# Kernel optimization log

Hardware: AMD Instinct MI355X
Metric: run time of the kernel (lower is better)

Reference implementation:

```python
import jax, jax.numpy as jnp
import numpy as np

N_HEADS = 16
ROPE_BASE = 10000.0
EPS = float(np.finfo(np.float32).eps)  # F.rms_norm default eps for fp32


def _rms_norm(x):
    # RMSNorm over last dim, no learned scale (modded-nanogpt `norm`)
    return x * jax.lax.rsqrt(jnp.mean(jnp.square(x), axis=-1, keepdims=True) + EPS)


def _rotary(x):
    # x: [B, T, H, D]; non-interleaved half-rotation as in the Rotary module
    B, T, H, D = x.shape
    inv_freq = (1.0 / ROPE_BASE) ** (jnp.arange(0, D, 2, dtype=jnp.float32) / D)  # [D/2]
    t = jnp.arange(T, dtype=jnp.float32)
    freqs = jnp.outer(t, inv_freq)  # [T, D/2]
    cos = jnp.cos(freqs)[None, :, None, :]
    sin = jnp.sin(freqs)[None, :, None, :]
    x1, x2 = jnp.split(x, 2, axis=3)
    y1 = x1 * cos + x2 * sin
    y2 = -x1 * sin + x2 * cos
    return jnp.concatenate((y1, y2), axis=3).astype(x.dtype)


def setup_inputs() -> dict:
    key = jax.random.key(0)
    k1, k2, k3, k4 = jax.random.split(key, 4)
    B, T, Hs = 1, 2048, 2048
    d_head = Hs // N_HEADS
    std = 0.5 * d_head ** (-0.5)
    bound = 3 ** 0.5 * std
    x = jax.random.normal(k1, (B, T, Hs), dtype=jnp.float32)
    Wqkv = jax.random.uniform(k2, (3, Hs, Hs), dtype=jnp.float32, minval=-bound, maxval=bound)
    Wo_w = jax.random.normal(k3, (Hs, Hs), dtype=jnp.float32) * (Hs ** -0.5)
    Wo_b = jax.random.normal(k4, (Hs,), dtype=jnp.float32) * 0.01
    return {"x": x, "Wqkv": Wqkv, "Wo_w": Wo_w, "Wo_b": Wo_b}


def reference(x, Wqkv, Wo_w, Wo_b):
    B, T, Hs = x.shape
    d_head = Hs // N_HEADS
    # fused QKV projection: F.linear(x, Wqkv.flatten(end_dim=1)) -> x @ W^T
    W = Wqkv.reshape(3 * Hs, Hs)
    qkv = jnp.einsum('bth,oh->bto', x, W).reshape(B, T, 3 * N_HEADS, d_head)
    q, k, v = jnp.split(qkv, 3, axis=-2)  # each [B, T, H, D]
    q, k = _rms_norm(q), _rms_norm(k)
    q, k = _rotary(q), _rotary(k)
    # causal attention (flex_attention block_mask = causal), scale = 1/sqrt(d)
    scale = 1.0 / jnp.sqrt(jnp.float32(d_head))
    scores = jnp.einsum('bthd,bshd->bhts', q, k) * scale  # [B, H, T, S]
    causal = jnp.tril(jnp.ones((T, T), dtype=bool))
    scores = jnp.where(causal[None, None], scores, jnp.float32(-1e30))
    probs = jax.nn.softmax(scores, axis=-1)
    y = jnp.einsum('bhts,bshd->bthd', probs, v).reshape(B, T, Hs)
    return jnp.einsum('bth,oh->bto', y, Wo_w) + Wo_b
```

## Files before the change

kernel.cpp:

```cpp
#include <hip/hip_runtime.h>
#include <hip/hip_bf16.h>
#include <stdint.h>

#define T_SEQ 2048
#define HS    2048
#define NH    16
#define DH    128
#define QKVN  (3*HS)

typedef __attribute__((ext_vector_type(8))) short          bf16x8;
typedef __attribute__((ext_vector_type(4))) float          f32x4;
typedef __attribute__((ext_vector_type(4))) unsigned short us4;
typedef __attribute__((ext_vector_type(8))) unsigned short us8;

__device__ __forceinline__ unsigned short f2bf(float x) {
  unsigned int u = __float_as_uint(x);
  return (unsigned short)((u + 0x7fffu + ((u >> 16) & 1u)) >> 16);
}

__device__ __forceinline__ void gl_lds16(const void* g, void* l) {
  __builtin_amdgcn_global_load_lds((__attribute__((address_space(1))) void*)g,
                                   (__attribute__((address_space(3))) void*)l, 16, 0, 0);
}

__global__ __launch_bounds__(256) void cast_bf16_kernel(const float* __restrict__ in,
                                                        unsigned short* __restrict__ out, int n) {
  int i = (blockIdx.x * 256 + threadIdx.x) * 8;
  if (i >= n) return;
  f32x4 a = *(const f32x4*)(in + i);
  f32x4 b = *(const f32x4*)(in + i + 4);
  us8 r;
#pragma unroll
  for (int j = 0; j < 4; ++j) { r[j] = f2bf(a[j]); r[j + 4] = f2bf(b[j]); }
  *(us8*)(out + i) = r;
}

__global__ __launch_bounds__(256) void rope_table_kernel(float* __restrict__ cosd,
                                                         float* __restrict__ sind) {
  int i = blockIdx.x * 256 + threadIdx.x;
  if (i >= T_SEQ * 64) return;
  int t = i >> 6, f = i & 63;
  float inv = expf(-9.210340371976184f * (float)f * (1.0f / 64.0f));
  float ang = (float)t * inv;
  float s, c;
  sincosf(ang, &s, &c);
  cosd[i] = c; sind[i] = s;
}

template <int BIAS, int BN>
__global__ __launch_bounds__(256, 4)
void gemm_bt(const unsigned short* __restrict__ A, const unsigned short* __restrict__ Bt,
             float* __restrict__ C, const float* __restrict__ bias, int M, int N, int K) {
  constexpr int FN = BN / 32;
  __shared__ unsigned short As[128 * 64];
  __shared__ unsigned short Bs[BN * 64];
  const int tid  = threadIdx.x;
  const int lane = tid & 63;
  const int w    = tid >> 6;
  const int fr   = lane & 15;
  const int fq   = lane >> 4;
  const int bm   = blockIdx.y * 128;
  const int bn   = blockIdx.x * BN;
  const int wr   = (w >> 1) * 64;
  const int wc   = (w & 1) * (BN / 2);

  f32x4 acc[4][FN];
#pragma unroll
  for (int m = 0; m < 4; ++m)
#pragma unroll
    for (int n = 0; n < FN; ++n) { acc[m][n][0]=0.f; acc[m][n][1]=0.f; acc[m][n][2]=0.f; acc[m][n][3]=0.f; }

  const int srow = lane >> 3;
  const int sg   = (lane & 7) ^ srow;
  const unsigned short* Ag = A + (long)bm * K;
  const unsigned short* Bg = Bt + (long)bn * K;

  const int nk = K >> 6;
  for (int kt = 0; kt < nk; ++kt) {
    const int k0 = kt << 6;
    __syncthreads();
#pragma unroll
    for (int i = 0; i < 4; ++i) {
      int r = i * 32 + w * 8;
      gl_lds16(Ag + (long)(r + srow) * K + k0 + sg * 8, &As[r * 64]);
    }
#pragma unroll
    for (int i = 0; i < BN / 32; ++i) {
      int r = i * 32 + w * 8;
      gl_lds16(Bg + (long)(r + srow) * K + k0 + sg * 8, &Bs[r * 64]);
    }
    __syncthreads();
    __builtin_amdgcn_s_setprio(1);
#pragma unroll
    for (int ks = 0; ks < 2; ++ks) {
      bf16x8 af[4], bfr[FN];
#pragma unroll
      for (int m = 0; m < 4; ++m)
        af[m]  = *(const bf16x8*)&As[(wr + m * 16 + fr) * 64 + (((ks * 4 + fq) ^ (fr & 7)) << 3)];
#pragma unroll
      for (int n = 0; n < FN; ++n)
        bfr[n] = *(const bf16x8*)&Bs[(wc + n * 16 + fr) * 64 + (((ks * 4 + fq) ^ (fr & 7)) << 3)];
#pragma unroll
      for (int m = 0; m < 4; ++m)
#pragma unroll
        for (int n = 0; n < FN; ++n)
          acc[m][n] = __builtin_amdgcn_mfma_f32_16x16x32_bf16(af[m], bfr[n], acc[m][n], 0, 0, 0);
    }
    __builtin_amdgcn_s_setprio(0);
  }
#pragma unroll
  for (int m = 0; m < 4; ++m) {
    int row0 = bm + wr + m * 16 + fq * 4;
#pragma unroll
    for (int n = 0; n < FN; ++n) {
      int col = bn + wc + n * 16 + fr;
      float bv = BIAS ? bias[col] : 0.0f;
#pragma unroll
      for (int j = 0; j < 4; ++j)
        C[(long)(row0 + j) * N + col] = acc[m][n][j] + bv;
    }
  }
}

__global__ __launch_bounds__(256)
void normrope_qk(const float* __restrict__ qkv, const float* __restrict__ cosd,
                 const float* __restrict__ sind, unsigned short* __restrict__ qb,
                 unsigned short* __restrict__ kb) {
  const int wgl  = (blockIdx.x * 256 + threadIdx.x) >> 6;
  const int lane = threadIdx.x & 63;
  for (int rr = wgl; rr < T_SEQ * 32; rr += 4096) {
    const int t = rr >> 5;
    const int y = rr & 31;
    const float2 v = *(const float2*)(qkv + (long)t * QKVN + y * 128 + lane * 2);
    float ss = v.x * v.x + v.y * v.y;
#pragma unroll
    for (int m = 1; m < 64; m <<= 1) ss += __shfl_xor(ss, m, 64);
    const float r = rsqrtf(ss * (1.0f / 128.0f) + 1.1920928955078125e-07f);
    const float a = v.x * r, b = v.y * r;
    const float pa = __shfl_xor(a, 32, 64), pb = __shfl_xor(b, 32, 64);
    const float2 c2 = *(const float2*)(cosd + t * 64 + (lane & 31) * 2);
    const float2 s2 = *(const float2*)(sind + t * 64 + (lane & 31) * 2);
    float o0, o1;
    if (lane < 32) { o0 =  a * c2.x + pa * s2.x;  o1 =  b * c2.y + pb * s2.y; }
    else           { o0 = -pa * s2.x + a * c2.x;  o1 = -pb * s2.y + b * c2.y; }
    unsigned short* dst = (y >> 4) ? kb : qb;
    const unsigned int packed = (unsigned int)f2bf(o0) | ((unsigned int)f2bf(o1) << 16);
    *(unsigned int*)(dst + ((long)(y & 15) * T_SEQ + t) * 128 + lane * 2) = packed;
  }
}

__global__ __launch_bounds__(256)
void v_transpose(const float* __restrict__ qkv, unsigned short* __restrict__ vt) {
  const int tb = blockIdx.x;
  const int h  = blockIdx.y;
  __shared__ unsigned short vl[128][72];
  const int tid = threadIdx.x;
#pragma unroll
  for (int p = 0; p < 32; ++p) {
    int rr = p * 2 + (tid >> 7);
    int d  = tid & 127;
    float x = qkv[(long)(tb * 64 + rr) * QKVN + 2 * HS + h * 128 + d];
    vl[d][rr] = f2bf(x);
  }
  __syncthreads();
#pragma unroll
  for (int p = 0; p < 8; ++p) {
    int idx = (p * 256 + tid) * 4;
    int d = idx >> 6;
    int i = idx & 63;
    us4 val = *(const us4*)&vl[d][i];
    *(us4*)&vt[((long)h * DH + d) * T_SEQ + tb * 64 + i] = val;
  }
}

__global__ __launch_bounds__(256, 2)
void attn_kernel(const unsigned short* __restrict__ qg, const unsigned short* __restrict__ kg,
                 const unsigned short* __restrict__ vtg, float* __restrict__ accG,
                 float* __restrict__ mlG) {
  const int bi = blockIdx.x;
  const int q0 = (bi & 255) >> 4;
  const int h  = bi & 15;
  const int quarter = bi >> 8;
  const int qb = (quarter < 2) ? (31 - q0) : q0;
  const int p  = quarter & 1;
  const int slot = (qb * 16 + h) * 2 + p;

  const int kt0 = p ? ((qb >> 1) + 1) : 0;
  const int kte = p ? qb : (qb >> 1);

  const int tid = threadIdx.x, lane = tid & 63, w = tid >> 6;
  const int fr = lane & 15, fq = lane >> 4;

  float* accO = accG + (long)slot * 8192;
  float* mlO  = mlG + slot * 128;

  if (kt0 > kte) {
#pragma unroll
    for (int j3 = 0; j3 < 4; ++j3) {
      int row = w * 16 + fq * 4 + j3;
      if (fr == 0) { mlO[row] = -1e30f; mlO[64 + row] = 0.f; }
    }
    return;
  }

  __shared__ unsigned short Ks[2][64 * 128];
  __shared__ unsigned short Vts[2][128 * 64];
  __shared__ unsigned short Ps[4][16 * 72];

  const unsigned short* qh = qg  + (long)h * T_SEQ * 128;
  const unsigned short* kh = kg  + (long)h * T_SEQ * 128;
  const unsigned short* vh = vtg + (long)h * 128 * T_SEQ;

  const int krow_off = lane >> 4;
  const int vrow_off = lane >> 3;
  const int vg       = (lane & 7) ^ vrow_off;

  {
    const unsigned short* ksrc = kh + (long)kt0 * 8192;
#pragma unroll
    for (int i = 0; i < 4; ++i) {
      int c = w * 4 + i;
      int r = 4 * c + krow_off;
      int gr = (lane & 15) ^ (r & 7);
      gl_lds16(ksrc + r * 128 + gr * 8, &Ks[0][c * 512]);
    }
#pragma unroll
    for (int i = 0; i < 4; ++i) {
      int r0 = (w * 4 + i) * 8;
      gl_lds16(vh + (long)(r0 + vrow_off) * T_SEQ + kt0 * 64 + vg * 8, &Vts[0][r0 * 64]);
    }
  }

  bf16x8 aq[4];
  {
    const unsigned short* qrow = qh + (long)(qb * 64 + w * 16 + fr) * 128;
#pragma unroll
    for (int ks = 0; ks < 4; ++ks)
      aq[ks] = *(const bf16x8*)(qrow + ks * 32 + fq * 8);
  }

  f32x4 acc[8];
#pragma unroll
  for (int n = 0; n < 8; ++n) { acc[n][0]=0.f; acc[n][1]=0.f; acc[n][2]=0.f; acc[n][3]=0.f; }
  float mrow[4], lrow[4];
#pragma unroll
  for (int j2 = 0; j2 < 4; ++j2) { mrow[j2] = -1e30f; lrow[j2] = 0.f; }

  const float scale = 0.08838834764831845f;

  __syncthreads();

  for (int kt = kt0; kt <= kte; ++kt) {
    const int cur = (kt - kt0) & 1;

    if (kt < kte) {
      const int nb = cur ^ 1;
      const unsigned short* ksrc = kh + (long)(kt + 1) * 8192;
#pragma unroll
      for (int i = 0; i < 4; ++i) {
        int c = w * 4 + i;
        int r = 4 * c + krow_off;
        int gr = (lane & 15) ^ (r & 7);
        gl_lds16(ksrc + r * 128 + gr * 8, &Ks[nb][c * 512]);
      }
#pragma unroll
      for (int i = 0; i < 4; ++i) {
        int r0 = (w * 4 + i) * 8;
        gl_lds16(vh + (long)(r0 + vrow_off) * T_SEQ + (kt + 1) * 64 + vg * 8, &Vts[nb][r0 * 64]);
      }
    }

    f32x4 sv[4];
#pragma unroll
    for (int n = 0; n < 4; ++n) { sv[n][0]=0.f; sv[n][1]=0.f; sv[n][2]=0.f; sv[n][3]=0.f; }
    __builtin_amdgcn_s_setprio(1);
#pragma unroll
    for (int ks = 0; ks < 4; ++ks)
#pragma unroll
      for (int n = 0; n < 4; ++n) {
        int R = n * 16 + fr;
        bf16x8 bk = *(const bf16x8*)&Ks[cur][R * 128 + (((ks * 4 + fq) ^ (fr & 7)) << 3)];
        sv[n] = __builtin_amdgcn_mfma_f32_16x16x32_bf16(aq[ks], bk, sv[n], 0, 0, 0);
      }
    __builtin_amdgcn_s_setprio(0);

#pragma unroll
    for (int n = 0; n < 4; ++n)
#pragma unroll
      for (int j3 = 0; j3 < 4; ++j3) {
        float s = sv[n][j3] * scale;
        if (kt == qb && (n * 16 + fr) > (w * 16 + fq * 4 + j3)) s = -1e30f;
        sv[n][j3] = s;
      }

    float pm[4];
#pragma unroll
    for (int j3 = 0; j3 < 4; ++j3)
      pm[j3] = fmaxf(fmaxf(sv[0][j3], sv[1][j3]), fmaxf(sv[2][j3], sv[3][j3]));
#pragma unroll
    for (int m = 1; m < 16; m <<= 1)
#pragma unroll
      for (int j3 = 0; j3 < 4; ++j3) pm[j3] = fmaxf(pm[j3], __shfl_xor(pm[j3], m, 64));

    float alpha[4];
#pragma unroll
    for (int j3 = 0; j3 < 4; ++j3) {
      float mn = fmaxf(mrow[j3], pm[j3]);
      alpha[j3] = __expf(mrow[j3] - mn);
      mrow[j3] = mn;
    }
    float rs[4] = {0.f, 0.f, 0.f, 0.f};
#pragma unroll
    for (int n = 0; n < 4; ++n)
#pragma unroll
      for (int j3 = 0; j3 < 4; ++j3) {
        float pval = __expf(sv[n][j3] - mrow[j3]);
        sv[n][j3] = pval;
        rs[j3] += pval;
      }
#pragma unroll
    for (int m = 1; m < 16; m <<= 1)
#pragma unroll
      for (int j3 = 0; j3 < 4; ++j3) rs[j3] += __shfl_xor(rs[j3], m, 64);
#pragma unroll
    for (int j3 = 0; j3 < 4; ++j3) lrow[j3] = lrow[j3] * alpha[j3] + rs[j3];
#pragma unroll
    for (int n = 0; n < 8; ++n)
#pragma unroll
      for (int j3 = 0; j3 < 4; ++j3) acc[n][j3] *= alpha[j3];

    unsigned short* pl = &Ps[w][0];
#pragma unroll
    for (int n = 0; n < 4; ++n)
#pragma unroll
      for (int j3 = 0; j3 < 4; ++j3)
        pl[(fq * 4 + j3) * 72 + n * 16 + fr] = f2bf(sv[n][j3]);
    asm volatile("s_waitcnt lgkmcnt(0)" ::: "memory");
    __builtin_amdgcn_s_setprio(1);
#pragma unroll
    for (int ks = 0; ks < 2; ++ks) {
      bf16x8 pa = *(const bf16x8*)&pl[fr * 72 + ks * 32 + fq * 8];
#pragma unroll
      for (int n = 0; n < 8; ++n) {
        int R = n * 16 + fr;
        bf16x8 bv = *(const bf16x8*)&Vts[cur][R * 64 + (((ks * 4 + fq) ^ (fr & 7)) << 3)];
        acc[n] = __builtin_amdgcn_mfma_f32_16x16x32_bf16(pa, bv, acc[n], 0, 0, 0);
      }
    }
    __builtin_amdgcn_s_setprio(0);

    __syncthreads();
  }

#pragma unroll
  for (int j3 = 0; j3 < 4; ++j3) {
    int row = w * 16 + fq * 4 + j3;
#pragma unroll
    for (int n = 0; n < 8; ++n)
      accO[row * 128 + n * 16 + fr] = acc[n][j3];
    if (fr == 0) { mlO[row] = mrow[j3]; mlO[64 + row] = lrow[j3]; }
  }
}

__global__ __launch_bounds__(256)
void attn_combine(const float* __restrict__ accG, const float* __restrict__ mlG,
                  unsigned short* __restrict__ yb) {
  const int j = blockIdx.x;
  const int qb = j >> 4, h = j & 15;
  const float* a0 = accG + (long)(j * 2 + 0) * 8192;
  const float* a1 = accG + (long)(j * 2 + 1) * 8192;
  const float* ml0 = mlG + (j * 2 + 0) * 128;
  const float* ml1 = mlG + (j * 2 + 1) * 128;
  const int tid = threadIdx.x;
#pragma unroll
  for (int e = 0; e < 8; ++e) {
    int idx = e * 256 + tid;
    int row = idx >> 5;
    int c4  = (idx & 31) * 4;
    float m0 = ml0[row], l0 = ml0[64 + row];
    float m1 = ml1[row], l1 = ml1[64 + row];
    float m  = fmaxf(m0, m1);
    float w0 = __expf(m0 - m), w1 = __expf(m1 - m);
    float inv = 1.0f / (l0 * w0 + l1 * w1);
    f32x4 A = *(const f32x4*)(a0 + row * 128 + c4);
    f32x4 B = *(const f32x4*)(a1 + row * 128 + c4);
    us4 o;
#pragma unroll
    for (int q = 0; q < 4; ++q)
      o[q] = f2bf((A[q] * w0 + B[q] * w1) * inv);
    *(us4*)(yb + (long)(qb * 64 + row) * HS + h * 128 + c4) = o;
  }
}

extern "C" void kernel_launch(void* const* d_in, const int* in_sizes, int n_in,
                              void* d_out, int out_size, void* d_ws, size_t ws_size,
                              hipStream_t stream) {
  const float* x    = (const float*)d_in[0];
  const float* Wqkv = (const float*)d_in[1];
  const float* Wo_w = (const float*)d_in[2];
  const float* Wo_b = (const float*)d_in[3];
  float* out = (float*)d_out;
  char* ws = (char*)d_ws;

  unsigned short* xbf  = (unsigned short*)(ws + 0L);
  unsigned short* wqbf = (unsigned short*)(ws + 8388608L);
  unsigned short* wobf = (unsigned short*)(ws + 33554432L);
  float*          qkv  = (float*)         (ws + 41943040L);
  unsigned short* qb   = (unsigned short*)(ws + 92274688L);
  unsigned short* kb   = (unsigned short*)(ws + 100663296L);
  unsigned short* vt   = (unsigned short*)(ws + 109051904L);
  unsigned short* yb   = (unsigned short*)(ws + 117440512L);
  float*          cosd = (float*)         (ws + 125829120L);
  float*          sind = (float*)         (ws + 126353408L);
  float*          accG = (float*)         (ws + 0L);
  float*          mlG  = (float*)         (ws + 41943040L);

  cast_bf16_kernel<<<dim3(4194304 / 8 / 256), 256, 0, stream>>>(x, xbf, 4194304);
  cast_bf16_kernel<<<dim3(12582912 / 8 / 256), 256, 0, stream>>>(Wqkv, wqbf, 12582912);
  cast_bf16_kernel<<<dim3(4194304 / 8 / 256), 256, 0, stream>>>(Wo_w, wobf, 4194304);
  rope_table_kernel<<<dim3(512), 256, 0, stream>>>(cosd, sind);

  gemm_bt<0, 128><<<dim3(QKVN / 128, T_SEQ / 128), 256, 0, stream>>>(xbf, wqbf, qkv, nullptr,
                                                                     T_SEQ, QKVN, HS);
  normrope_qk<<<dim3(1024), 256, 0, stream>>>(qkv, cosd, sind, qb, kb);
  v_transpose<<<dim3(T_SEQ / 64, NH), 256, 0, stream>>>(qkv, vt);
  attn_kernel<<<dim3(1024), 256, 0, stream>>>(qb, kb, vt, accG, mlG);
  attn_combine<<<dim3(512), 256, 0, stream>>>(accG, mlG, yb);
  gemm_bt<1, 64><<<dim3(HS / 64, T_SEQ / 128), 256, 0, stream>>>(yb, wobf, out, Wo_b,
                                                                 T_SEQ, HS, HS);
}
```

Before: 289.1 us.

## Compute softmax row sums via MFMA, use exp2, skip rescale when max unchanged

Folds log2(e) into the score scale so every exponential becomes exp2f, and the combine kernel now uses base-2 weights to match. The row-sum shuffle reduction is replaced by an extra MFMA of the bf16 probabilities against a vector of ones, accumulating the normalizer in accS. The acc/alpha rescaling is wrapped in a wave-uniform branch that runs only when some row max grows. This removes shuffle reductions and VALU work from the softmax inner loop, at the cost of an extra MFMA per k-step and a normalizer summed from bf16-rounded probabilities.

```diff
diff --git a/kernel.cpp b/kernel.cpp
--- a/kernel.cpp
+++ b/kernel.cpp
@@ -239,14 +239,19 @@
       aq[ks] = *(const bf16x8*)(qrow + ks * 32 + fq * 8);
   }
 
+  bf16x8 vone;
+#pragma unroll
+  for (int e = 0; e < 8; ++e) vone[e] = (short)0x3F80;
+
   f32x4 acc[8];
 #pragma unroll
   for (int n = 0; n < 8; ++n) { acc[n][0]=0.f; acc[n][1]=0.f; acc[n][2]=0.f; acc[n][3]=0.f; }
-  float mrow[4], lrow[4];
-#pragma unroll
-  for (int j2 = 0; j2 < 4; ++j2) { mrow[j2] = -1e30f; lrow[j2] = 0.f; }
-
-  const float scale = 0.08838834764831845f;
+  f32x4 accS;  accS[0]=0.f; accS[1]=0.f; accS[2]=0.f; accS[3]=0.f;
+  float mrow[4];
+#pragma unroll
+  for (int j2 = 0; j2 < 4; ++j2) mrow[j2] = -1e30f;
+
+  const float scale2 = 0.08838834764831845f * 1.4426950408889634f;
 
   __syncthreads();
 
@@ -288,7 +293,7 @@
     for (int n = 0; n < 4; ++n)
 #pragma unroll
       for (int j3 = 0; j3 < 4; ++j3) {
-        float s = sv[n][j3] * scale;
+        float s = sv[n][j3] * scale2;
         if (kt == qb && (n * 16 + fr) > (w * 16 + fq * 4 + j3)) s = -1e30f;
         sv[n][j3] = s;
       }
@@ -302,44 +307,35 @@
 #pragma unroll
       for (int j3 = 0; j3 < 4; ++j3) pm[j3] = fmaxf(pm[j3], __shfl_xor(pm[j3], m, 64));
 
-    float alpha[4];
-#pragma unroll
-    for (int j3 = 0; j3 < 4; ++j3) {
-      float mn = fmaxf(mrow[j3], pm[j3]);
-      alpha[j3] = __expf(mrow[j3] - mn);
-      mrow[j3] = mn;
-    }
-    float rs[4] = {0.f, 0.f, 0.f, 0.f};
+    bool grow = (pm[0] > mrow[0]) | (pm[1] > mrow[1]) | (pm[2] > mrow[2]) | (pm[3] > mrow[3]);
+    if (__any(grow)) {
+      float alpha[4];
+#pragma unroll
+      for (int j3 = 0; j3 < 4; ++j3) {
+        float mn = fmaxf(mrow[j3], pm[j3]);
+        alpha[j3] = exp2f(mrow[j3] - mn);
+        mrow[j3] = mn;
+      }
+#pragma unroll
+      for (int n = 0; n < 8; ++n)
+#pragma unroll
+        for (int j3 = 0; j3 < 4; ++j3) acc[n][j3] *= alpha[j3];
+#pragma unroll
+      for (int j3 = 0; j3 < 4; ++j3) accS[j3] *= alpha[j3];
+    }
+
+    unsigned short* pl = &Ps[w][0];
 #pragma unroll
     for (int n = 0; n < 4; ++n)
 #pragma unroll
-      for (int j3 = 0; j3 < 4; ++j3) {
-        float pval = __expf(sv[n][j3] - mrow[j3]);
-        sv[n][j3] = pval;
-        rs[j3] += pval;
-      }
-#pragma unroll
-    for (int m = 1; m < 16; m <<= 1)
-#pragma unroll
-      for (int j3 = 0; j3 < 4; ++j3) rs[j3] += __shfl_xor(rs[j3], m, 64);
-#pragma unroll
-    for (int j3 = 0; j3 < 4; ++j3) lrow[j3] = lrow[j3] * alpha[j3] + rs[j3];
-#pragma unroll
-    for (int n = 0; n < 8; ++n)
-#pragma unroll
-      for (int j3 = 0; j3 < 4; ++j3) acc[n][j3] *= alpha[j3];
-
-    unsigned short* pl = &Ps[w][0];
-#pragma unroll
-    for (int n = 0; n < 4; ++n)
-#pragma unroll
       for (int j3 = 0; j3 < 4; ++j3)
-        pl[(fq * 4 + j3) * 72 + n * 16 + fr] = f2bf(sv[n][j3]);
+        pl[(fq * 4 + j3) * 72 + n * 16 + fr] = f2bf(exp2f(sv[n][j3] - mrow[j3]));
     asm volatile("s_waitcnt lgkmcnt(0)" ::: "memory");
     __builtin_amdgcn_s_setprio(1);
 #pragma unroll
     for (int ks = 0; ks < 2; ++ks) {
       bf16x8 pa = *(const bf16x8*)&pl[fr * 72 + ks * 32 + fq * 8];
+      accS = __builtin_amdgcn_mfma_f32_16x16x32_bf16(pa, vone, accS, 0, 0, 0);
 #pragma unroll
       for (int n = 0; n < 8; ++n) {
         int R = n * 16 + fr;
@@ -358,7 +354,7 @@
 #pragma unroll
     for (int n = 0; n < 8; ++n)
       accO[row * 128 + n * 16 + fr] = acc[n][j3];
-    if (fr == 0) { mlO[row] = mrow[j3]; mlO[64 + row] = lrow[j3]; }
+    if (fr == 0) { mlO[row] = mrow[j3]; mlO[64 + row] = accS[j3]; }
   }
 }
 
@@ -380,7 +376,7 @@
     float m0 = ml0[row], l0 = ml0[64 + row];
     float m1 = ml1[row], l1 = ml1[64 + row];
     float m  = fmaxf(m0, m1);
-    float w0 = __expf(m0 - m), w1 = __expf(m1 - m);
+    float w0 = exp2f(m0 - m), w1 = exp2f(m1 - m);
     float inv = 1.0f / (l0 * w0 + l1 * w1);
     f32x4 A = *(const f32x4*)(a0 + row * 128 + c4);
     f32x4 B = *(const f32x4*)(a1 + row * 128 + c4);
```

New measurement: 296.2 us. 2.5% more time.
